# Kernel tuning notes

Hardware: AMD Instinct MI355X
Metric: run time of the kernel (lower is better)

## Reference

```python
import jax, jax.numpy as jnp
import numpy as np


def setup_inputs() -> dict:
    V, D, E = 4096, 128, 12288
    key = jax.random.key(0)
    k1, k2, k3 = jax.random.split(key, 3)
    features = jax.random.normal(k1, (V, D), dtype=jnp.float32)
    # random self-loop-free edge list
    v0 = jax.random.randint(k2, (E,), 0, V)
    off = jax.random.randint(k3, (E,), 1, V)
    v1 = (v0 + off) % V
    edges = jnp.stack([v0, v1]).astype(jnp.int32)  # [2, E]
    # manifold-style neighbor matrix: interior edges share 2 faces
    neighbor = (jnp.zeros((V, V), jnp.int32)
                .at[edges[0], edges[1]].set(2)
                .at[edges[1], edges[0]].set(2))
    return {"features": features, "edges": edges, "neighbor": neighbor}


def _collapse(features, edges, neighbor):
    """Greedy heap-order edge collapse. The heap is built once and only popped,
    so pop order == edges sorted by priority ||f[v0]||^2 + ||f[v1]||^2.
    Returns merge matrix A (f_out = A @ f_in), alive vertex mask, final count."""
    V = neighbor.shape[0]
    target = jnp.int32(V // 2)
    pri = jnp.sum(features * features, axis=1)          # [V]
    epri = pri[edges[0]] + pri[edges[1]]                # [E]
    order = jnp.argsort(epri)                           # heappop order (stable ties)
    alive0 = jnp.ones((V,), bool)
    A0 = jnp.eye(V, dtype=jnp.float32)
    cnt0 = jnp.int32(V)

    def step(carry, e):
        alive, n, A, cnt = carry
        v0 = edges[0, e]
        v1 = edges[1, e]
        do = (cnt > target) & alive[v0] & alive[v1] & (n[v0, v1] == 2)
        # merged neighbor row for v0; v1 dies
        r = (n[v0] + n[v1]).at[v0].set(0).at[v1].set(0)
        row0 = jnp.where(do, r, n[v0])
        row1 = jnp.where(do, jnp.zeros_like(r), n[v1])
        n = (n.at[v0, :].set(row0).at[:, v0].set(row0)
              .at[v1, :].set(row1).at[:, v1].set(row1))
        arow = jnp.where(do, 0.5 * (A[v0] + A[v1]), A[v0])
        A = A.at[v0].set(arow)
        alive = alive.at[v1].set(alive[v1] & jnp.logical_not(do))
        cnt = cnt - do.astype(jnp.int32)
        return (alive, n, A, cnt), None

    (alive, n, A, cnt), _ = jax.lax.scan(step, (alive0, neighbor, A0, cnt0), order)
    return A, alive, cnt


def reference(features, edges, neighbor):
    edges = edges.astype(jnp.int32)
    A, alive, cnt = _collapse(features, edges, neighbor)
    # clean_up() compacts removed vertices; under jit we mask dead rows instead
    pooled = (A @ features) * alive[:, None].astype(features.dtype)
    return pooled, alive, cnt
```

## Files before the change

### kernel.cpp

```cpp
#include <hip/hip_runtime.h>
#include <stdint.h>

#define V 4096
#define D 128
#define E 12288
#define NPAD 16384
#define HALF 8192
#define TARGET 2048
#define MAXM (V - TARGET)
#define ROWU32 256
#define CAP 32

#define WAIT_VM0   0x0F70

#define WS_N      0u
#define WS_PRI    (V * ROWU32 * 4u)
#define WS_KEYS   (WS_PRI + V * 4u)
#define WS_PK     (WS_KEYS + NPAD * 8u)
#define WS_PAIRS  (WS_PK + E * 4u)
#define WS_MCOUNT (WS_PAIRS + MAXM * 4u)
#define WS_ALIVE  (WS_MCOUNT + 16u)

typedef const __attribute__((address_space(1))) unsigned* gas1_t;
typedef __attribute__((address_space(3))) unsigned* las3_t;

__device__ __forceinline__ unsigned getf(const uint4& r, int c) {
    unsigned lo = (c & 2) ? r.z : r.x;
    unsigned hi = (c & 2) ? r.w : r.y;
    return (c & 1) ? hi : lo;
}
__device__ __forceinline__ void andf(uint4& r, int c, unsigned msk) {
    if (c == 0) r.x &= msk; else if (c == 1) r.y &= msk;
    else if (c == 2) r.z &= msk; else r.w &= msk;
}

__global__ void k_scatter(const int* __restrict__ edges, unsigned* __restrict__ n32) {
    int e = blockIdx.x * 256 + threadIdx.x;
    if (e < E) {
        int a = edges[e], b = edges[E + e];
        atomicOr(&n32[a * ROWU32 + (b >> 4)], 2u << ((b & 15) * 2));
        atomicOr(&n32[b * ROWU32 + (a >> 4)], 2u << ((a & 15) * 2));
    }
}

__global__ void k_pri(const float* __restrict__ f, float* __restrict__ pri) {
    int v = blockIdx.x * 256 + threadIdx.x;
    if (v < V) {
        const float* p = f + v * D;
        float r[8];
#pragma unroll
        for (int j = 0; j < 8; j++) r[j] = __fmul_rn(p[j], p[j]);
        for (int i = 8; i < D; i += 8) {
#pragma unroll
            for (int j = 0; j < 8; j++)
                r[j] = __fadd_rn(r[j], __fmul_rn(p[i + j], p[i + j]));
        }
        float s01 = __fadd_rn(r[0], r[1]);
        float s23 = __fadd_rn(r[2], r[3]);
        float s45 = __fadd_rn(r[4], r[5]);
        float s67 = __fadd_rn(r[6], r[7]);
        pri[v] = __fadd_rn(__fadd_rn(s01, s23), __fadd_rn(s45, s67));
    }
}

__global__ void k_keys(const int* __restrict__ edges, const float* __restrict__ pri,
                       unsigned long long* __restrict__ keys) {
    int s = blockIdx.x * 256 + threadIdx.x;
    if (s < NPAD) {
        unsigned long long rec;
        if (s < E) {
            int a = edges[s], b = edges[E + s];
            float k = __fadd_rn(pri[a], pri[b]);
            rec = ((unsigned long long)__float_as_uint(k) << 32) | (unsigned)s;
        } else {
            rec = (0xFFFFFFFFull << 32) | (unsigned)s;
        }
        keys[s] = rec;
    }
}

__launch_bounds__(1024)
__global__ void k_sort2(unsigned long long* __restrict__ keys) {
    __shared__ unsigned long long srt[HALF];
    const int tid = threadIdx.x;
    unsigned long long* base = keys + blockIdx.x * HALF;
    for (int s = tid; s < HALF; s += 1024) srt[s] = base[s];
    __syncthreads();
    for (int k = 2; k <= HALF; k <<= 1) {
        for (int j = k >> 1; j >= 1; j >>= 1) {
            for (int i = tid; i < HALF; i += 1024) {
                int ixj = i ^ j;
                if (ixj > i) {
                    unsigned long long x = srt[i], y = srt[ixj];
                    bool up = ((i & k) == 0);
                    if ((x > y) == up) { srt[i] = y; srt[ixj] = x; }
                }
            }
            __syncthreads();
        }
    }
    for (int s = tid; s < HALF; s += 1024) base[s] = srt[s];
}

__launch_bounds__(64)
__global__ void k_mergepath(const unsigned long long* __restrict__ keys,
                            const int* __restrict__ edges, unsigned* __restrict__ pkG) {
    int t = blockIdx.x * 64 + threadIdx.x;
    if (t >= E / 64) return;
    const unsigned long long* A = keys;
    const unsigned long long* B = keys + HALF;
    int d = t * 64;
    int lo = d > HALF ? d - HALF : 0;
    int hi = d < HALF ? d : HALF;
    while (lo < hi) {
        int mid = (lo + hi) >> 1;
        if (A[mid] < B[d - 1 - mid]) lo = mid + 1; else hi = mid;
    }
    int ia = lo, ib = d - lo;
    for (int o = d; o < d + 64; o++) {
        bool takeA = (ib >= HALF) || (ia < HALF && A[ia] < B[ib]);
        unsigned long long r = takeA ? A[ia++] : B[ib++];
        int e = (int)(r & 0xFFFFFFFFull);
        int a = edges[e], b = edges[E + e];
        pkG[o] = ((unsigned)a << 16) | (unsigned)b;
    }
}

__launch_bounds__(64, 1)
__global__ void k_collapse(const unsigned* __restrict__ pkG, unsigned* n32,
                           unsigned* __restrict__ pairsG, int* __restrict__ mcountG,
                           uint8_t* __restrict__ aliveG, float* __restrict__ out) {
    __shared__ unsigned shRows[2 * CAP * ROWU32];
    __shared__ uint8_t  alive[V];
    __shared__ unsigned shCand[CAP];
    __shared__ unsigned shConf[CAP];
    __shared__ unsigned shDeadM[CAP];
    const int lane = threadIdx.x;
    for (int v = lane; v < V; v += 64) alive[v] = 1;
    __syncthreads();

    int cnt = V, mcount = 0, head = 64;
    unsigned pkv = pkG[lane];
    unsigned fv = 0u;
    bool fknown = false;
    bool dec = false;

    while (true) {
        const int a = (int)(pkv >> 16), b = (int)(pkv & 0xFFFFu);
        if (!dec && !(alive[a] && alive[b])) dec = true;
        bool unk = !dec && !fknown;
        bool drained = false;
        if (__ballot(unk)) {
            __builtin_amdgcn_s_waitcnt(WAIT_VM0);
            drained = true;
            if (unk) {
                unsigned wv = *(volatile unsigned*)(n32 + a * ROWU32 + (b >> 4));
                fv = (wv >> ((b & 15) * 2)) & 3u;
                fknown = true;
            }
        }
        if (!dec && fv != 2u) dec = true;
        unsigned long long mF = __ballot(!dec);

        if (mF) {
            int limit = cnt - TARGET; if (limit > CAP) limit = CAP;
            int flagged = (int)__popcll(mF);
            int nacc = flagged < limit ? flagged : limit;

            int myK = -1;
            if (!dec) {
                int rank = (int)__popcll(mF & ((1ull << lane) - 1ull));
                if (rank < limit) { myK = rank; shCand[rank] = pkv; }
            }
            if (lane < CAP) { shConf[lane] = 0u; shDeadM[lane] = 0u; }
            __syncthreads();

            if (!drained) __builtin_amdgcn_s_waitcnt(WAIT_VM0);
            for (int k = 0; k < nacc; k++) {
                unsigned cp = shCand[k];
                int v0 = (int)(cp >> 16), v1 = (int)(cp & 0xFFFFu);
                __builtin_amdgcn_global_load_lds(
                    (gas1_t)(n32 + v0 * ROWU32 + lane * 4),
                    (las3_t)(shRows + (2 * k) * ROWU32), 16, 0, 0);
                __builtin_amdgcn_global_load_lds(
                    (gas1_t)(n32 + v1 * ROWU32 + lane * 4),
                    (las3_t)(shRows + (2 * k + 1) * ROWU32), 16, 0, 0);
            }
            __builtin_amdgcn_s_waitcnt(WAIT_VM0);
            __syncthreads();

            for (int pp = lane; pp < CAP * CAP; pp += 64) {
                int k = pp >> 5, j = pp & 31;
                if (j < k && k < nacc) {
                    unsigned cj = shCand[j], ck = shCand[k];
                    int v0j = (int)(cj >> 16), v1j = (int)(cj & 0xFFFFu);
                    int v0k = (int)(ck >> 16), v1k = (int)(ck & 0xFFFFu);
                    bool dkill = (v0k == v1j) || (v1k == v1j);
                    bool c = dkill || (v0k == v0j) || (v1k == v0j);
                    const unsigned* rBj = shRows + (2 * j + 1) * ROWU32;
                    const unsigned* rBk = shRows + (2 * k + 1) * ROWU32;
                    c |= ((rBj[v0k >> 4] >> ((v0k & 15) * 2)) & 3u) != 0u;
                    c |= ((rBj[v1k >> 4] >> ((v1k & 15) * 2)) & 3u) != 0u;
                    c |= ((rBk[v0j >> 4] >> ((v0j & 15) * 2)) & 3u) != 0u;
                    if (c) atomicOr(&shConf[k], 1u << j);
                    if (dkill) atomicOr(&shDeadM[k], 1u << j);
                }
            }
            __syncthreads();

            unsigned kept = 0u, blocked = 0u, deadm = 0u;
            for (int k = 0; k < nacc; k++) {
                unsigned bit = 1u << k;
                if (shDeadM[k] & kept) { deadm |= bit; continue; }
                if (shConf[k] & (kept | blocked)) { blocked |= bit; continue; }
                kept |= bit;
            }
            int nk = __popc(kept);
            if (myK >= 0 && (((kept | deadm) >> myK) & 1u)) dec = true;

            if (lane < nacc && ((kept >> lane) & 1u)) {
                unsigned cp = shCand[lane];
                alive[(int)(cp & 0xFFFFu)] = 0;
                int r = __popc(kept & ((1u << lane) - 1u));
                pairsG[mcount + r] = cp;
            }
            mcount += nk; cnt -= nk;
            __syncthreads();
            if (cnt == TARGET) break;

            {
                int g = lane >> 1, sub = lane & 1;
                if (g < nacc && ((kept >> g) & 1u)) {
                    unsigned cp = shCand[g];
                    int v0 = (int)(cp >> 16), v1 = (int)(cp & 0xFFFFu);
                    const uint4* rowA = (const uint4*)(shRows + (2 * g) * ROWU32);
                    const uint4* rowB = (const uint4*)(shRows + (2 * g + 1) * ROWU32);
                    int m0u = v0 >> 6, m1u = v1 >> 6;
                    int sh0 = (v0 & 15) * 2, wi0 = v0 >> 4;
                    for (int t = 0; t < 32; t++) {
                        int u = sub * 32 + ((t + lane) & 31);
                        uint4 ra = rowA[u], rb = rowB[u];
                        uint4 rr;
                        rr.x = ra.x | rb.x | ((ra.x & rb.x & 0xAAAAAAAAu) >> 1);
                        rr.y = ra.y | rb.y | ((ra.y & rb.y & 0xAAAAAAAAu) >> 1);
                        rr.z = ra.z | rb.z | ((ra.z & rb.z & 0xAAAAAAAAu) >> 1);
                        rr.w = ra.w | rb.w | ((ra.w & rb.w & 0xAAAAAAAAu) >> 1);
                        if (u == m0u) andf(rr, (v0 >> 4) & 3, ~(3u << ((v0 & 15) * 2)));
                        if (u == m1u) andf(rr, (v1 >> 4) & 3, ~(3u << ((v1 & 15) * 2)));
                        ((uint4*)(n32 + v0 * ROWU32))[u] = rr;
#pragma unroll
                        for (int c = 0; c < 4; c++) {
                            unsigned bb = getf(rb, c);
                            if (!bb) continue;
                            unsigned aa = getf(ra, c), vvv = getf(rr, c);
                            int xbase = (u << 6) + (c << 4);
                            unsigned tt = bb;
                            while (tt) {
                                int q = (__ffs(tt) - 1) >> 1;
                                tt &= ~(3u << (q * 2));
                                int x = xbase + q;
                                if (x != v0 && x != v1) {
                                    unsigned dx =
                                        (((aa >> (q*2)) ^ (vvv >> (q*2))) & 3u) << sh0;
                                    if (dx) atomicXor(n32 + x * ROWU32 + wi0, dx);
                                }
                            }
                        }
                    }
                }
            }
            __syncthreads();

            if (!dec && fknown) {
                unsigned km = kept;
                while (km) {
                    int j = __ffs(km) - 1; km &= km - 1u;
                    int v0j = (int)(shCand[j] >> 16);
                    if (a == v0j || b == v0j) { fknown = false; break; }
                }
            }
            __syncthreads();
        } else {
            if (head >= E) break;
        }

        {
            unsigned long long mU = __ballot(!dec);
            int nU = (int)__popcll(mU);
            int p = 0;
#pragma unroll
            for (int step = 32; step; step >>= 1) {
                int cand = p + step;
                unsigned long long pref =
                    (cand >= 64) ? ~0ull : ((1ull << cand) - 1ull);
                if ((int)__popcll(mU & pref) <= lane) p = cand;
            }
            unsigned npkv = (unsigned)__shfl((int)pkv, p);
            unsigned nfv  = (unsigned)__shfl((int)fv, p);
            int      nfk  = __shfl((int)fknown, p);
            if (lane < nU) {
                pkv = npkv; fv = nfv; fknown = (nfk != 0); dec = false;
            } else {
                int idx = head + lane - nU;
                if (idx < E) { pkv = pkG[idx]; fknown = false; dec = false; }
                else dec = true;
            }
            head += 64 - nU;
        }
    }

    for (int v = lane; v < V; v += 64) {
        uint8_t ao = alive[v];
        aliveG[v] = ao;
        out[V * D + v] = ao ? 1.0f : 0.0f;
    }
    if (lane == 0) { mcountG[0] = mcount; out[V * D + V] = (float)cnt; }
}

__launch_bounds__(256)
__global__ void k_apply(const float* __restrict__ f, const unsigned* __restrict__ pairsG,
                        const int* __restrict__ mcountG, float* __restrict__ out) {
    __shared__ unsigned pl[MAXM];
    __shared__ int rootL[256];
    __shared__ float wL[256];
    const int tid = threadIdx.x;
    const int mc = mcountG[0];
    for (int j = tid; j < mc; j += 256) pl[j] = pairsG[j];
    __syncthreads();
    int cur = blockIdx.x * 256 + tid;
    float w = 1.0f;
    for (int j = 0; j < mc; j++) {
        unsigned p = pl[j];
        int v0 = (int)(p >> 16), v1 = (int)(p & 0xFFFFu);
        if (cur == v1) { cur = v0; w *= 0.5f; }
        else if (cur == v0) w *= 0.5f;
    }
    rootL[tid] = cur;
    wL[tid] = w;
    __syncthreads();
    const int sub = tid >> 7;
    const int d = tid & 127;
    for (int s = 0; s < 256; s += 2) {
        int idx = s + sub;
        int vv = blockIdx.x * 256 + idx;
        atomicAdd(&out[rootL[idx] * D + d], wL[idx] * f[vv * D + d]);
    }
}

extern "C" void kernel_launch(void* const* d_in, const int* in_sizes, int n_in,
                              void* d_out, int out_size, void* d_ws, size_t ws_size,
                              hipStream_t stream) {
    (void)in_sizes; (void)n_in; (void)out_size; (void)ws_size;
    const float* features = (const float*)d_in[0];
    const int* edges = (const int*)d_in[1];
    uint8_t* ws = (uint8_t*)d_ws;
    unsigned* n32 = (unsigned*)(ws + WS_N);
    float* pri = (float*)(ws + WS_PRI);
    unsigned long long* keys = (unsigned long long*)(ws + WS_KEYS);
    unsigned* pkG = (unsigned*)(ws + WS_PK);
    unsigned* pairsG = (unsigned*)(ws + WS_PAIRS);
    int* mcountG = (int*)(ws + WS_MCOUNT);
    uint8_t* aliveG = ws + WS_ALIVE;
    float* out = (float*)d_out;

    hipMemsetAsync(n32, 0, (size_t)V * ROWU32 * 4, stream);
    hipMemsetAsync(out, 0, (size_t)V * D * sizeof(float), stream);
    k_pri<<<(V + 255) / 256, 256, 0, stream>>>(features, pri);
    k_scatter<<<(E + 255) / 256, 256, 0, stream>>>(edges, n32);
    k_keys<<<(NPAD + 255) / 256, 256, 0, stream>>>(edges, pri, keys);
    k_sort2<<<2, 1024, 0, stream>>>(keys);
    k_mergepath<<<(E / 64 + 63) / 64, 64, 0, stream>>>(keys, edges, pkG);
    k_collapse<<<1, 64, 0, stream>>>(pkG, n32, pairsG, mcountG, aliveG, out);
    k_apply<<<V / 256, 256, 0, stream>>>(features, pairsG, mcountG, out);
}
```

Before: 3.818 ms.

## Process candidate batch sequentially in LDS with deduped rows and deferred global XOR log

Replaces the pairwise conflict matrix with a sequential per-candidate loop. Each step re-checks eligibility against LDS-resident rows and merges rows in shared memory. Distinct endpoint rows are deduplicated through a vertex-to-slot map, and column updates to other vertices are logged and flushed to global memory with atomics after the batch, so more candidates per batch can be accepted. It also drops the cached face-value state in favour of always re-reading the neighbor word. The cost is more barriers per kept edge and a bounded log that may overflow.

```diff
diff --git a/kernel.cpp b/kernel.cpp
--- a/kernel.cpp
+++ b/kernel.cpp
@@ -10,6 +10,7 @@
 #define MAXM (V - TARGET)
 #define ROWU32 256
 #define CAP 32
+#define LOGCAP 4096
 
 #define WAIT_VM0   0x0F70
 
@@ -130,156 +131,165 @@
 __global__ void k_collapse(const unsigned* __restrict__ pkG, unsigned* n32,
                            unsigned* __restrict__ pairsG, int* __restrict__ mcountG,
                            uint8_t* __restrict__ aliveG, float* __restrict__ out) {
-    __shared__ unsigned shRows[2 * CAP * ROWU32];
+    __shared__ unsigned shRows[64 * ROWU32];
     __shared__ uint8_t  alive[V];
+    __shared__ uint8_t  shV2S[V];
     __shared__ unsigned shCand[CAP];
-    __shared__ unsigned shConf[CAP];
-    __shared__ unsigned shDeadM[CAP];
+    __shared__ unsigned shLog[LOGCAP];
+    __shared__ int      shLogN;
     const int lane = threadIdx.x;
-    for (int v = lane; v < V; v += 64) alive[v] = 1;
+    for (int v = lane; v < V; v += 64) { alive[v] = 1; shV2S[v] = 0xFF; }
     __syncthreads();
 
     int cnt = V, mcount = 0, head = 64;
     unsigned pkv = pkG[lane];
-    unsigned fv = 0u;
-    bool fknown = false;
     bool dec = false;
 
     while (true) {
         const int a = (int)(pkv >> 16), b = (int)(pkv & 0xFFFFu);
         if (!dec && !(alive[a] && alive[b])) dec = true;
-        bool unk = !dec && !fknown;
-        bool drained = false;
-        if (__ballot(unk)) {
-            __builtin_amdgcn_s_waitcnt(WAIT_VM0);
-            drained = true;
-            if (unk) {
-                unsigned wv = *(volatile unsigned*)(n32 + a * ROWU32 + (b >> 4));
-                fv = (wv >> ((b & 15) * 2)) & 3u;
-                fknown = true;
-            }
-        }
-        if (!dec && fv != 2u) dec = true;
+        __builtin_amdgcn_s_waitcnt(WAIT_VM0);
+        if (!dec) {
+            unsigned wv = *(volatile unsigned*)(n32 + a * ROWU32 + (b >> 4));
+            if (((wv >> ((b & 15) * 2)) & 3u) != 2u) dec = true;
+        }
         unsigned long long mF = __ballot(!dec);
 
+        int ev = -1;
         if (mF) {
-            int limit = cnt - TARGET; if (limit > CAP) limit = CAP;
             int flagged = (int)__popcll(mF);
-            int nacc = flagged < limit ? flagged : limit;
-
+            int nacc = flagged < CAP ? flagged : CAP;
             int myK = -1;
             if (!dec) {
                 int rank = (int)__popcll(mF & ((1ull << lane) - 1ull));
-                if (rank < limit) { myK = rank; shCand[rank] = pkv; }
-            }
-            if (lane < CAP) { shConf[lane] = 0u; shDeadM[lane] = 0u; }
-            __syncthreads();
-
-            if (!drained) __builtin_amdgcn_s_waitcnt(WAIT_VM0);
-            for (int k = 0; k < nacc; k++) {
-                unsigned cp = shCand[k];
-                int v0 = (int)(cp >> 16), v1 = (int)(cp & 0xFFFFu);
-                __builtin_amdgcn_global_load_lds(
-                    (gas1_t)(n32 + v0 * ROWU32 + lane * 4),
-                    (las3_t)(shRows + (2 * k) * ROWU32), 16, 0, 0);
-                __builtin_amdgcn_global_load_lds(
-                    (gas1_t)(n32 + v1 * ROWU32 + lane * 4),
-                    (las3_t)(shRows + (2 * k + 1) * ROWU32), 16, 0, 0);
+                if (rank < CAP) { myK = rank; shCand[rank] = pkv; }
+            }
+            if (lane == 0) shLogN = 0;
+            __syncthreads();
+
+            if (lane < 2 * nacc) {
+                unsigned cp = shCand[lane >> 1];
+                ev = (lane & 1) ? (int)(cp & 0xFFFFu) : (int)(cp >> 16);
+                shV2S[ev] = (uint8_t)lane;
+            }
+            __syncthreads();
+            bool primary = (ev >= 0) && (shV2S[ev] == (uint8_t)lane);
+            {
+                unsigned long long mm = __ballot(primary);
+                while (mm) {
+                    int s = __ffsll((long long)mm) - 1; mm &= mm - 1ull;
+                    int vv = __shfl(ev, s);
+                    __builtin_amdgcn_global_load_lds(
+                        (gas1_t)(n32 + vv * ROWU32 + lane * 4),
+                        (las3_t)(shRows + s * ROWU32), 16, 0, 0);
+                }
             }
             __builtin_amdgcn_s_waitcnt(WAIT_VM0);
             __syncthreads();
 
-            for (int pp = lane; pp < CAP * CAP; pp += 64) {
-                int k = pp >> 5, j = pp & 31;
-                if (j < k && k < nacc) {
-                    unsigned cj = shCand[j], ck = shCand[k];
-                    int v0j = (int)(cj >> 16), v1j = (int)(cj & 0xFFFFu);
-                    int v0k = (int)(ck >> 16), v1k = (int)(ck & 0xFFFFu);
-                    bool dkill = (v0k == v1j) || (v1k == v1j);
-                    bool c = dkill || (v0k == v0j) || (v1k == v0j);
-                    const unsigned* rBj = shRows + (2 * j + 1) * ROWU32;
-                    const unsigned* rBk = shRows + (2 * k + 1) * ROWU32;
-                    c |= ((rBj[v0k >> 4] >> ((v0k & 15) * 2)) & 3u) != 0u;
-                    c |= ((rBj[v1k >> 4] >> ((v1k & 15) * 2)) & 3u) != 0u;
-                    c |= ((rBk[v0j >> 4] >> ((v0j & 15) * 2)) & 3u) != 0u;
-                    if (c) atomicOr(&shConf[k], 1u << j);
-                    if (dkill) atomicOr(&shDeadM[k], 1u << j);
-                }
-            }
-            __syncthreads();
-
-            unsigned kept = 0u, blocked = 0u, deadm = 0u;
-            for (int k = 0; k < nacc; k++) {
-                unsigned bit = 1u << k;
-                if (shDeadM[k] & kept) { deadm |= bit; continue; }
-                if (shConf[k] & (kept | blocked)) { blocked |= bit; continue; }
-                kept |= bit;
-            }
-            int nk = __popc(kept);
-            if (myK >= 0 && (((kept | deadm) >> myK) & 1u)) dec = true;
-
-            if (lane < nacc && ((kept >> lane) & 1u)) {
-                unsigned cp = shCand[lane];
-                alive[(int)(cp & 0xFFFFu)] = 0;
-                int r = __popc(kept & ((1u << lane) - 1u));
-                pairsG[mcount + r] = cp;
-            }
-            mcount += nk; cnt -= nk;
-            __syncthreads();
-            if (cnt == TARGET) break;
-
-            {
-                int g = lane >> 1, sub = lane & 1;
-                if (g < nacc && ((kept >> g) & 1u)) {
-                    unsigned cp = shCand[g];
+            const int limit = cnt - TARGET;
+            unsigned resid = (nacc >= 32) ? 0xFFFFFFFFu : ((1u << nacc) - 1u);
+            unsigned keptM = 0u;
+            int keptRound = 0;
+            while (resid && keptRound < limit) {
+                bool elig = false;
+                if (lane < nacc && ((resid >> lane) & 1u)) {
+                    unsigned cp = shCand[lane];
                     int v0 = (int)(cp >> 16), v1 = (int)(cp & 0xFFFFu);
-                    const uint4* rowA = (const uint4*)(shRows + (2 * g) * ROWU32);
-                    const uint4* rowB = (const uint4*)(shRows + (2 * g + 1) * ROWU32);
-                    int m0u = v0 >> 6, m1u = v1 >> 6;
-                    int sh0 = (v0 & 15) * 2, wi0 = v0 >> 4;
-                    for (int t = 0; t < 32; t++) {
-                        int u = sub * 32 + ((t + lane) & 31);
-                        uint4 ra = rowA[u], rb = rowB[u];
-                        uint4 rr;
-                        rr.x = ra.x | rb.x | ((ra.x & rb.x & 0xAAAAAAAAu) >> 1);
-                        rr.y = ra.y | rb.y | ((ra.y & rb.y & 0xAAAAAAAAu) >> 1);
-                        rr.z = ra.z | rb.z | ((ra.z & rb.z & 0xAAAAAAAAu) >> 1);
-                        rr.w = ra.w | rb.w | ((ra.w & rb.w & 0xAAAAAAAAu) >> 1);
-                        if (u == m0u) andf(rr, (v0 >> 4) & 3, ~(3u << ((v0 & 15) * 2)));
-                        if (u == m1u) andf(rr, (v1 >> 4) & 3, ~(3u << ((v1 & 15) * 2)));
-                        ((uint4*)(n32 + v0 * ROWU32))[u] = rr;
+                    if (alive[v0] && alive[v1]) {
+                        int sA = shV2S[v0];
+                        unsigned wv = shRows[sA * ROWU32 + (v1 >> 4)];
+                        elig = ((wv >> ((v1 & 15) * 2)) & 3u) == 2u;
+                    }
+                }
+                unsigned E32 = (unsigned)__ballot(elig);
+                resid &= E32;
+                if (!resid) break;
+                const int k = __ffs(resid) - 1;
+                resid &= ~(1u << k);
+                keptM |= 1u << k;
+                const unsigned cp = shCand[k];
+                const int v0 = (int)(cp >> 16), v1 = (int)(cp & 0xFFFFu);
+                const int sA = shV2S[v0], sB = shV2S[v1];
+                if (lane == 0) { alive[v1] = 0; pairsG[mcount] = cp; }
+                mcount++; keptRound++;
+                const uint4 ra = ((const uint4*)(shRows + sA * ROWU32))[lane];
+                const uint4 rb = ((const uint4*)(shRows + sB * ROWU32))[lane];
+                __syncthreads();
+                uint4 rr;
+                rr.x = ra.x | rb.x | ((ra.x & rb.x & 0xAAAAAAAAu) >> 1);
+                rr.y = ra.y | rb.y | ((ra.y & rb.y & 0xAAAAAAAAu) >> 1);
+                rr.z = ra.z | rb.z | ((ra.z & rb.z & 0xAAAAAAAAu) >> 1);
+                rr.w = ra.w | rb.w | ((ra.w & rb.w & 0xAAAAAAAAu) >> 1);
+                if ((v0 >> 6) == lane) andf(rr, (v0 >> 4) & 3, ~(3u << ((v0 & 15) * 2)));
+                if ((v1 >> 6) == lane) andf(rr, (v1 >> 4) & 3, ~(3u << ((v1 & 15) * 2)));
+                ((uint4*)(shRows + sA * ROWU32))[lane] = rr;
+                const int wi0 = v0 >> 4, sh0 = (v0 & 15) * 2;
 #pragma unroll
-                        for (int c = 0; c < 4; c++) {
-                            unsigned bb = getf(rb, c);
-                            if (!bb) continue;
-                            unsigned aa = getf(ra, c), vvv = getf(rr, c);
-                            int xbase = (u << 6) + (c << 4);
-                            unsigned tt = bb;
-                            while (tt) {
-                                int q = (__ffs(tt) - 1) >> 1;
-                                tt &= ~(3u << (q * 2));
-                                int x = xbase + q;
-                                if (x != v0 && x != v1) {
-                                    unsigned dx =
-                                        (((aa >> (q*2)) ^ (vvv >> (q*2))) & 3u) << sh0;
-                                    if (dx) atomicXor(n32 + x * ROWU32 + wi0, dx);
-                                }
+                for (int c = 0; c < 4; c++) {
+                    unsigned bb = getf(rb, c);
+                    if (!bb) continue;
+                    unsigned aa = getf(ra, c);
+                    int xbase = (lane << 6) + (c << 4);
+                    unsigned tt = bb;
+                    while (tt) {
+                        int q = (__ffs(tt) - 1) >> 1;
+                        tt &= ~(3u << (q * 2));
+                        int x = xbase + q;
+                        if (x != v0 && x != v1) {
+                            unsigned a2 = (aa >> (q * 2)) & 3u;
+                            unsigned b2 = (bb >> (q * 2)) & 3u;
+                            unsigned n2 = a2 | b2 | ((a2 & b2 & 2u) >> 1);
+                            unsigned dx = a2 ^ n2;
+                            if (dx) {
+                                int s = shV2S[x];
+                                if (s != 0xFF)
+                                    shRows[s * ROWU32 + wi0] ^= (dx << sh0);
+                                int li = atomicAdd(&shLogN, 1);
+                                if (li < LOGCAP)
+                                    shLog[li] = ((unsigned)x << 16) |
+                                                ((unsigned)k << 2) | dx;
                             }
                         }
                     }
                 }
-            }
-            __syncthreads();
-
-            if (!dec && fknown) {
-                unsigned km = kept;
+                __syncthreads();
+            }
+            if (myK >= 0 && !((resid >> myK) & 1u)) dec = true;
+            cnt -= keptRound;
+            __syncthreads();
+
+            {
+                unsigned km = keptM;
                 while (km) {
-                    int j = __ffs(km) - 1; km &= km - 1u;
-                    int v0j = (int)(shCand[j] >> 16);
-                    if (a == v0j || b == v0j) { fknown = false; break; }
-                }
-            }
-            __syncthreads();
+                    int k2 = __ffs(km) - 1; km &= km - 1u;
+                    int v0 = (int)(shCand[k2] >> 16);
+                    int s = shV2S[v0];
+                    ((uint4*)(n32 + v0 * ROWU32))[lane] =
+                        ((const uint4*)(shRows + s * ROWU32))[lane];
+                }
+                int ln = shLogN; if (ln > LOGCAP) ln = LOGCAP;
+                for (int e2 = lane; e2 < ln; e2 += 64) {
+                    unsigned ent = shLog[e2];
+                    int x = (int)(ent >> 16);
+                    int k2 = (int)((ent >> 2) & 31u);
+                    unsigned dx = ent & 3u;
+                    bool skip = false;
+                    unsigned km2 = keptM;
+                    while (km2) {
+                        int j = __ffs(km2) - 1; km2 &= km2 - 1u;
+                        if ((int)(shCand[j] >> 16) == x) { skip = true; break; }
+                    }
+                    if (!skip) {
+                        int v0 = (int)(shCand[k2] >> 16);
+                        atomicXor(n32 + x * ROWU32 + (v0 >> 4),
+                                  dx << ((v0 & 15) * 2));
+                    }
+                }
+            }
+            __syncthreads();
+            if (ev >= 0) shV2S[ev] = 0xFF;
+            if (cnt == TARGET) break;
         } else {
             if (head >= E) break;
         }
@@ -290,19 +300,16 @@
             int p = 0;
 #pragma unroll
             for (int step = 32; step; step >>= 1) {
-                int cand = p + step;
+                int c2 = p + step;
                 unsigned long long pref =
-                    (cand >= 64) ? ~0ull : ((1ull << cand) - 1ull);
-                if ((int)__popcll(mU & pref) <= lane) p = cand;
+                    (c2 >= 64) ? ~0ull : ((1ull << c2) - 1ull);
+                if ((int)__popcll(mU & pref) <= lane) p = c2;
             }
             unsigned npkv = (unsigned)__shfl((int)pkv, p);
-            unsigned nfv  = (unsigned)__shfl((int)fv, p);
-            int      nfk  = __shfl((int)fknown, p);
-            if (lane < nU) {
-                pkv = npkv; fv = nfv; fknown = (nfk != 0); dec = false;
-            } else {
+            if (lane < nU) { pkv = npkv; dec = false; }
+            else {
                 int idx = head + lane - nU;
-                if (idx < E) { pkv = pkG[idx]; fknown = false; dec = false; }
+                if (idx < E) { pkv = pkG[idx]; dec = false; }
                 else dec = true;
             }
             head += 64 - nU;
```

New measurement: 4.883 ms. 1.28x slower.

## Allow same-v0 chained collapses in one batch and merge them by group leader

Applied to the files above, without the earlier changes.

Candidates in a batch that share the same surviving vertex v0 no longer count as conflicts. They are tracked as a chain with extra dead and distance masks, so more collapses can be accepted per batch iteration. A leader lane per v0 group merges all of the group's v1 rows into one saturated row. It then propagates only the changed column bits to alive neighbours through atomic XOR. This cuts the number of serial batch iterations at the cost of more complex conflict logic, with a risk of diverging from the exact sequential semantics.

```diff
diff --git a/kernel.cpp b/kernel.cpp
--- a/kernel.cpp
+++ b/kernel.cpp
@@ -32,6 +32,14 @@
 __device__ __forceinline__ void andf(uint4& r, int c, unsigned msk) {
     if (c == 0) r.x &= msk; else if (c == 1) r.y &= msk;
     else if (c == 2) r.z &= msk; else r.w &= msk;
+}
+__device__ __forceinline__ uint4 satq(uint4 a, uint4 b) {
+    uint4 r;
+    r.x = a.x | b.x | ((a.x & b.x & 0xAAAAAAAAu) >> 1);
+    r.y = a.y | b.y | ((a.y & b.y & 0xAAAAAAAAu) >> 1);
+    r.z = a.z | b.z | ((a.z & b.z & 0xAAAAAAAAu) >> 1);
+    r.w = a.w | b.w | ((a.w & b.w & 0xAAAAAAAAu) >> 1);
+    return r;
 }
 
 __global__ void k_scatter(const int* __restrict__ edges, unsigned* __restrict__ n32) {
@@ -135,6 +143,8 @@
     __shared__ unsigned shCand[CAP];
     __shared__ unsigned shConf[CAP];
     __shared__ unsigned shDeadM[CAP];
+    __shared__ unsigned shChain[CAP];
+    __shared__ unsigned shDnz[CAP];
     const int lane = threadIdx.x;
     for (int v = lane; v < V; v += 64) alive[v] = 1;
     __syncthreads();
@@ -172,7 +182,10 @@
                 int rank = (int)__popcll(mF & ((1ull << lane) - 1ull));
                 if (rank < limit) { myK = rank; shCand[rank] = pkv; }
             }
-            if (lane < CAP) { shConf[lane] = 0u; shDeadM[lane] = 0u; }
+            if (lane < CAP) {
+                shConf[lane] = 0u; shDeadM[lane] = 0u;
+                shChain[lane] = 0u; shDnz[lane] = 0u;
+            }
             __syncthreads();
 
             if (!drained) __builtin_amdgcn_s_waitcnt(WAIT_VM0);
@@ -196,26 +209,41 @@
                     int v0j = (int)(cj >> 16), v1j = (int)(cj & 0xFFFFu);
                     int v0k = (int)(ck >> 16), v1k = (int)(ck & 0xFFFFu);
                     bool dkill = (v0k == v1j) || (v1k == v1j);
-                    bool c = dkill || (v0k == v0j) || (v1k == v0j);
-                    const unsigned* rBj = shRows + (2 * j + 1) * ROWU32;
-                    const unsigned* rBk = shRows + (2 * k + 1) * ROWU32;
-                    c |= ((rBj[v0k >> 4] >> ((v0k & 15) * 2)) & 3u) != 0u;
-                    c |= ((rBj[v1k >> 4] >> ((v1k & 15) * 2)) & 3u) != 0u;
-                    c |= ((rBk[v0j >> 4] >> ((v0j & 15) * 2)) & 3u) != 0u;
-                    if (c) atomicOr(&shConf[k], 1u << j);
-                    if (dkill) atomicOr(&shDeadM[k], 1u << j);
+                    if (dkill) {
+                        atomicOr(&shDeadM[k], 1u << j);
+                        atomicOr(&shConf[k], 1u << j);
+                    } else if (v0j == v0k) {
+                        atomicOr(&shChain[k], 1u << j);
+                        const unsigned* rBj = shRows + (2 * j + 1) * ROWU32;
+                        unsigned d = (rBj[v1k >> 4] >> ((v1k & 15) * 2)) & 3u;
+                        if (d) atomicOr(&shDnz[k], 1u << j);
+                    } else {
+                        bool c = (v1k == v0j);
+                        const unsigned* rBj = shRows + (2 * j + 1) * ROWU32;
+                        const unsigned* rBk = shRows + (2 * k + 1) * ROWU32;
+                        c |= ((rBj[v0k >> 4] >> ((v0k & 15) * 2)) & 3u) != 0u;
+                        c |= ((rBj[v1k >> 4] >> ((v1k & 15) * 2)) & 3u) != 0u;
+                        c |= ((rBk[v0j >> 4] >> ((v0j & 15) * 2)) & 3u) != 0u;
+                        if (c) atomicOr(&shConf[k], 1u << j);
+                    }
                 }
             }
             __syncthreads();
 
             unsigned kept = 0u, blocked = 0u, deadm = 0u;
-            for (int k = 0; k < nacc; k++) {
+            int m = 0;
+#pragma unroll
+            for (int k = 0; k < CAP; k++) {
+                if (k >= nacc) continue;
                 unsigned bit = 1u << k;
-                if (shDeadM[k] & kept) { deadm |= bit; continue; }
-                if (shConf[k] & (kept | blocked)) { blocked |= bit; continue; }
-                kept |= bit;
-            }
-            int nk = __popc(kept);
+                unsigned dead = shDeadM[k], chain = shChain[k];
+                unsigned dnz = shDnz[k], conf = shConf[k];
+                if ((dead & kept) || (chain & kept & dnz)) { deadm |= bit; continue; }
+                if ((conf & (kept | blocked)) || (chain & blocked)) {
+                    blocked |= bit; continue;
+                }
+                kept |= bit; m++;
+            }
             if (myK >= 0 && (((kept | deadm) >> myK) & 1u)) dec = true;
 
             if (lane < nacc && ((kept >> lane) & 1u)) {
@@ -224,7 +252,7 @@
                 int r = __popc(kept & ((1u << lane) - 1u));
                 pairsG[mcount + r] = cp;
             }
-            mcount += nk; cnt -= nk;
+            mcount += m; cnt -= m;
             __syncthreads();
             if (cnt == TARGET) break;
 
@@ -232,37 +260,56 @@
                 int g = lane >> 1, sub = lane & 1;
                 if (g < nacc && ((kept >> g) & 1u)) {
                     unsigned cp = shCand[g];
-                    int v0 = (int)(cp >> 16), v1 = (int)(cp & 0xFFFFu);
-                    const uint4* rowA = (const uint4*)(shRows + (2 * g) * ROWU32);
-                    const uint4* rowB = (const uint4*)(shRows + (2 * g + 1) * ROWU32);
-                    int m0u = v0 >> 6, m1u = v1 >> 6;
-                    int sh0 = (v0 & 15) * 2, wi0 = v0 >> 4;
-                    for (int t = 0; t < 32; t++) {
-                        int u = sub * 32 + ((t + lane) & 31);
-                        uint4 ra = rowA[u], rb = rowB[u];
-                        uint4 rr;
-                        rr.x = ra.x | rb.x | ((ra.x & rb.x & 0xAAAAAAAAu) >> 1);
-                        rr.y = ra.y | rb.y | ((ra.y & rb.y & 0xAAAAAAAAu) >> 1);
-                        rr.z = ra.z | rb.z | ((ra.z & rb.z & 0xAAAAAAAAu) >> 1);
-                        rr.w = ra.w | rb.w | ((ra.w & rb.w & 0xAAAAAAAAu) >> 1);
-                        if (u == m0u) andf(rr, (v0 >> 4) & 3, ~(3u << ((v0 & 15) * 2)));
-                        if (u == m1u) andf(rr, (v1 >> 4) & 3, ~(3u << ((v1 & 15) * 2)));
-                        ((uint4*)(n32 + v0 * ROWU32))[u] = rr;
+                    const int v0 = (int)(cp >> 16);
+                    unsigned grpM = 0u;
+                    {
+                        unsigned km = kept;
+                        while (km) {
+                            int kk = __ffs(km) - 1; km &= km - 1u;
+                            if ((int)(shCand[kk] >> 16) == v0) grpM |= 1u << kk;
+                        }
+                    }
+                    bool leader = ((grpM & ((1u << g) - 1u)) == 0u);
+                    if (leader) {
+                        const int wi0 = v0 >> 4;
+                        const unsigned sh0 = (unsigned)((v0 & 15) * 2);
+                        for (int t = 0; t < 32; t++) {
+                            int u = sub * 32 + ((t + lane) & 31);
+                            uint4 orig = ((const uint4*)(shRows + (2*g) * ROWU32))[u];
+                            uint4 q = orig;
+                            unsigned mm = grpM;
+                            while (mm) {
+                                int kk = __ffs(mm) - 1; mm &= mm - 1u;
+                                q = satq(q, ((const uint4*)
+                                             (shRows + (2*kk+1) * ROWU32))[u]);
+                            }
+                            if ((v0 >> 6) == u)
+                                andf(q, (v0 >> 4) & 3, ~(3u << ((v0 & 15) * 2)));
+                            mm = grpM;
+                            while (mm) {
+                                int kk = __ffs(mm) - 1; mm &= mm - 1u;
+                                int v1k = (int)(shCand[kk] & 0xFFFFu);
+                                if ((v1k >> 6) == u)
+                                    andf(q, (v1k >> 4) & 3,
+                                         ~(3u << ((v1k & 15) * 2)));
+                            }
+                            ((uint4*)(n32 + v0 * ROWU32))[u] = q;
+                            uint4 dq;
+                            dq.x = orig.x ^ q.x; dq.y = orig.y ^ q.y;
+                            dq.z = orig.z ^ q.z; dq.w = orig.w ^ q.w;
 #pragma unroll
-                        for (int c = 0; c < 4; c++) {
-                            unsigned bb = getf(rb, c);
-                            if (!bb) continue;
-                            unsigned aa = getf(ra, c), vvv = getf(rr, c);
-                            int xbase = (u << 6) + (c << 4);
-                            unsigned tt = bb;
-                            while (tt) {
-                                int q = (__ffs(tt) - 1) >> 1;
-                                tt &= ~(3u << (q * 2));
-                                int x = xbase + q;
-                                if (x != v0 && x != v1) {
-                                    unsigned dx =
-                                        (((aa >> (q*2)) ^ (vvv >> (q*2))) & 3u) << sh0;
-                                    if (dx) atomicXor(n32 + x * ROWU32 + wi0, dx);
+                            for (int c2 = 0; c2 < 4; c2++) {
+                                unsigned dd = getf(dq, c2);
+                                if (!dd) continue;
+                                int xbase = (u << 6) + (c2 << 4);
+                                while (dd) {
+                                    int qq = (__ffs(dd) - 1) >> 1;
+                                    unsigned dx = (dd >> (qq * 2)) & 3u;
+                                    dd &= ~(3u << (qq * 2));
+                                    int x = xbase + qq;
+                                    if (x != v0 && alive[x])
+                                        atomicXor(n32 + x * ROWU32 + wi0,
+                                                  dx << sh0);
                                 }
                             }
                         }
```

Result: slower. 4.943 ms (+29.5%).
